# Kernel optimization log

Hardware: AMD Instinct MI355X
Metric: run time of the kernel (lower is better)

The kernel has to match this reference:

```python
import jax, jax.numpy as jnp
import numpy as np

B, N_CLS, A = 2, 3, 3
D = H = W = 96
K = 128
ALPHA = 1.0
EPS = 1e-4
BETA = 1.0 / 9
LAMB1 = LAMB2 = LAMB3 = 1.0


def setup_inputs() -> dict:
    key = jax.random.key(0)
    k1, k2, k3, k4, k5, k6, k7, k8 = jax.random.split(key, 8)
    cls_logit = jax.random.normal(k1, (B, N_CLS * A, D, H, W), jnp.float32)
    reg_pred = jax.random.normal(k2, (B, 6 * A, D, H, W), jnp.float32)

    def make_coord(ka, kd):
        ca = jax.random.randint(ka, (B, K, 1), 0, A)
        cs = jax.random.randint(kd, (B, K, 3), 0, D)
        c = jnp.concatenate([ca, cs], -1).astype(jnp.int32)
        valid = (jnp.arange(K) < (3 * K // 4))[None, :, None]
        return jnp.where(valid, c, -1)

    coord_prob = make_coord(k3, k4)
    coord_diff = make_coord(k5, k6)
    # class labels 1..N_CLS scattered into prob_gt at the positive coords; -1 elsewhere = negative
    cls_lab = jax.random.randint(k7, (B, K), 1, N_CLS + 1).astype(jnp.float32)
    prob_gt = -jnp.ones((B, A, D, H, W), jnp.float32)
    bidx = jnp.broadcast_to(jnp.arange(B)[:, None], (B, K))
    cc = jnp.maximum(coord_prob, 0)
    lab = jnp.where(coord_prob[:, :, 0] > -1, cls_lab, -1.0)
    prob_gt = prob_gt.at[bidx, cc[..., 0], cc[..., 1], cc[..., 2], cc[..., 3]].set(lab)
    diff_gt = jax.random.normal(k8, (B, K, 6), jnp.float32) * 0.1
    weight_cls = jnp.array([1.0, 2.0, 1.5], jnp.float32)  # [1] + cls_weight
    return {"cls_logit": cls_logit, "reg_pred": reg_pred, "prob_gt": prob_gt,
            "coord_prob": coord_prob, "coord_diff": coord_diff,
            "diff_gt": diff_gt, "weight_cls": weight_cls}


def _gather(x, c):
    # x: [C, A, D, H, W], c: [K, 4] -> [C, K]
    return x[:, c[:, 0], c[:, 1], c[:, 2], c[:, 3]]


def _smooth_l1(x, t):
    n = jnp.abs(x - t)
    return jnp.where(n < BETA, 0.5 * n * n / BETA, n - 0.5 * BETA)


def _forward(cls_logit, reg_pred, diff_gt, weight_cls, prob_gt, coord_prob, coord_diff):
    sg = jax.lax.stop_gradient
    prob = jnp.clip(jax.nn.sigmoid(cls_logit), EPS, 1.0 - EPS)  # [B, NC*A, D, H, W]

    # ---- negative focal loss with NMS-style peak filtering ----
    negmask = jnp.broadcast_to((prob_gt == -1.0).astype(jnp.float32)[:, None],
                               (B, N_CLS, A, D, H, W)).reshape(B, N_CLS * A, D, H, W)
    mp = jax.lax.reduce_window(cls_logit, -jnp.inf, jax.lax.max,
                               (1, 1, 3, 3, 3), (1, 1, 1, 1, 1),
                               [(0, 0), (0, 0), (1, 1), (1, 1), (1, 1)])
    negmask = negmask * (mp == cls_logit).astype(jnp.float32) * (prob > EPS).astype(jnp.float32)
    w_neg = sg(prob) ** ALPHA * negmask
    l_neg = -jnp.sum(jnp.log(1.0 - prob) * w_neg)
    count_neg = jnp.sum(w_neg)

    # ---- positive focal loss (masked fixed-K gather replaces ragged per-sample loop) ----
    p6 = prob.reshape(B, N_CLS, A, D, H, W)
    mask = (coord_prob[:, :, 0] > -1).astype(jnp.float32)  # [B, K]
    cc = jnp.maximum(coord_prob, 0)
    p_others = jax.vmap(_gather)(p6, cc)  # [B, NC, K]
    pg = jax.vmap(lambda p, c: p[c[:, 0], c[:, 1], c[:, 2], c[:, 3]])(prob_gt, cc)
    cls_gt = jnp.clip(pg.astype(jnp.int32) - 1, 0, N_CLS - 1)  # [B, K]
    p_target = jnp.take_along_axis(p_others, cls_gt[:, None, :], axis=1)[:, 0]  # [B, K]
    w_pos = sg(1.0 - p_target) ** ALPHA * weight_cls[cls_gt] * mask
    l_pos = -jnp.sum(jnp.log(p_target) * w_pos)
    count_pos = jnp.sum(w_pos)

    # ---- other-class suppression term ----
    is_tgt = jnp.arange(N_CLS)[None, :, None] == cls_gt[:, None, :]
    w_oth = (jax.nn.relu(p_others - (p_target - 0.1)[:, None, :])
             * (p_others > 0.5) * (p_target > 0.5)[:, None, :])
    w_oth = sg(jnp.where(is_tgt, 0.0, w_oth) * mask[:, None, :])
    l_other = jnp.sum(-jnp.log(1.0 - p_others) * w_oth)
    count_other = jnp.sum(w_oth)

    d6 = reg_pred.reshape(B, 6, A, D, H, W)
    mask_d = (coord_diff[:, :, 0] > -1).astype(jnp.float32)
    ccd = jnp.maximum(coord_diff, 0)
    d_samp = jnp.transpose(jax.vmap(_gather)(d6, ccd), (0, 2, 1))  # [B, K, 6]
    reg_loss = jnp.sum(_smooth_l1(d_samp, diff_gt) * mask_d[:, :, None])
    reg_weight = jnp.sum(mask_d)

    total = l_pos + l_neg * LAMB1 + l_other * LAMB3 + reg_loss * LAMB2
    return jnp.stack([total, l_pos, l_neg, l_other, reg_loss,
                      count_pos, count_neg, count_other, reg_weight])


def reference(cls_logit, reg_pred, prob_gt, coord_prob, coord_diff, diff_gt, weight_cls):
    return _forward(cls_logit, reg_pred, diff_gt, weight_cls, prob_gt, coord_prob, coord_diff)
```

## Files before the change

### kernel.cpp

```cpp
#include <hip/hip_runtime.h>
#include <cmath>

constexpr int B_ = 2, NCLS = 3, A_ = 3, D_ = 96, H_ = 96, W_ = 96, K_ = 128;
constexpr int CH = NCLS * A_;
constexpr int HW = H_ * W_;
constexpr int SPAT = D_ * HW;
constexpr float EPS_ = 1e-4f;
constexpr float BETA_ = 1.0f / 9.0f;

constexpr int WPL = 6;
constexpr int DCHUNK = 6;
constexpr int NDC = D_ / DCHUNK;
constexpr int HGRP = 4;
constexpr int NHG = H_ / HGRP;
constexpr int NWAVES = B_ * CH * NHG * NDC;
constexpr int NBLK = NWAVES / 4;

static __device__ __forceinline__ float sigmoid_clip(float x) {
  float s = 1.0f / (1.0f + __expf(-x));
  return fminf(fmaxf(s, EPS_), 1.0f - EPS_);
}

static __device__ __forceinline__ void load6(const float* __restrict__ p,
                                             float* f) {
  const float2 u0 = *(const float2*)(p);
  const float2 u1 = *(const float2*)(p + 2);
  const float2 u2 = *(const float2*)(p + 4);
  f[0] = u0.x; f[1] = u0.y; f[2] = u1.x;
  f[3] = u1.y; f[4] = u2.x; f[5] = u2.y;
}

__global__ __launch_bounds__(256) void neg_loss_kernel(
    const float* __restrict__ x, const float* __restrict__ pgt,
    float* __restrict__ ws) {
  const int tid = threadIdx.x;
  const int lane = tid & 63;
  int t = blockIdx.x * 4 + (tid >> 6);
  const int dci = t % NDC; t /= NDC;
  const int hg = t % NHG; t /= NHG;
  const int c = t % CH;
  const int b = t / CH;

  const int hl = lane >> 4;
  const int wseg = lane & 15;
  const int h = hg * HGRP + hl;
  const int w0 = wseg * WPL;
  const int d0 = dci * DCHUNK;
  const int a = c - (c / A_) * A_;

  const float* base = x + (size_t)(b * CH + c) * SPAT;
  const int hm = max(h - 1, 0), hq = min(h + 1, H_ - 1);
  const float* rowm = base + hm * W_ + w0;
  const float* rowc = base + h * W_ + w0;
  const float* rowp = base + hq * W_ + w0;
  const float* pgb = pgt + (size_t)(b * A_ + a) * SPAT + h * W_ + w0;

  float sprev[6], scur[6], ccur[6];
  float bufm[2][6], bufc[2][6], bufp[2][6];
  float pgbuf[2][6];
  {
    float fm[6], fc[6], fp[6], gm[6], gc[6], gp[6];
    const int plm = max(d0 - 1, 0) * HW;
    load6(rowm + plm, fm); load6(rowc + plm, fc); load6(rowp + plm, fp);
    const int pl0 = d0 * HW;
    load6(rowm + pl0, gm); load6(rowc + pl0, gc); load6(rowp + pl0, gp);
    const int pl1 = (d0 + 1) * HW;
    load6(rowm + pl1, bufm[0]); load6(rowc + pl1, bufc[0]);
    load6(rowp + pl1, bufp[0]);
    const int pl2 = (d0 + 2) * HW;
    load6(rowm + pl2, bufm[1]); load6(rowc + pl2, bufc[1]);
    load6(rowp + pl2, bufp[1]);
    load6(pgb + pl0, pgbuf[0]);
    load6(pgb + pl1, pgbuf[1]);
#pragma unroll
    for (int i = 0; i < 6; ++i) sprev[i] = fmaxf(fmaxf(fm[i], fc[i]), fp[i]);
#pragma unroll
    for (int i = 0; i < 6; ++i) {
      scur[i] = fmaxf(fmaxf(gm[i], gc[i]), gp[i]);
      ccur[i] = gc[i];
    }
  }

  float lsum = 0.0f, csum = 0.0f;
#pragma unroll
  for (int k = 0; k < DCHUNK; ++k) {
    const int d = d0 + k;
    const int par = k & 1;
    float snext[6], cnext[6], pgc[6];
#pragma unroll
    for (int i = 0; i < 6; ++i) {
      snext[i] = fmaxf(fmaxf(bufm[par][i], bufc[par][i]), bufp[par][i]);
      cnext[i] = bufc[par][i];
      pgc[i] = pgbuf[par][i];
    }
    const int pl3 = min(d + 3, D_ - 1) * HW;
    load6(rowm + pl3, bufm[par]); load6(rowc + pl3, bufc[par]);
    load6(rowp + pl3, bufp[par]);
    load6(pgb + min(d + 2, D_ - 1) * HW, pgbuf[par]);

    float cmx[6], m[6];
#pragma unroll
    for (int i = 0; i < 6; ++i)
      cmx[i] = fmaxf(fmaxf(sprev[i], scur[i]), snext[i]);
    float left = __shfl_up(cmx[5], 1);
    float right = __shfl_down(cmx[0], 1);
    if (wseg == 0) left = cmx[0];
    if (wseg == 15) right = cmx[5];
    m[0] = fmaxf(left, fmaxf(cmx[0], cmx[1]));
    m[1] = fmaxf(cmx[0], fmaxf(cmx[1], cmx[2]));
    m[2] = fmaxf(cmx[1], fmaxf(cmx[2], cmx[3]));
    m[3] = fmaxf(cmx[2], fmaxf(cmx[3], cmx[4]));
    m[4] = fmaxf(cmx[3], fmaxf(cmx[4], cmx[5]));
    m[5] = fmaxf(cmx[4], fmaxf(cmx[5], right));

#pragma unroll
    for (int i = 0; i < 6; ++i) {
      const float prob = sigmoid_clip(ccur[i]);
      const bool pred =
          (m[i] == ccur[i]) && (pgc[i] == -1.0f) && (prob > EPS_);
      lsum += pred ? (-__logf(1.0f - prob) * prob) : 0.0f;
      csum += pred ? prob : 0.0f;
    }
#pragma unroll
    for (int i = 0; i < 6; ++i) {
      sprev[i] = scur[i]; scur[i] = snext[i]; ccur[i] = cnext[i];
    }
  }

#pragma unroll
  for (int off = 32; off > 0; off >>= 1) {
    lsum += __shfl_down(lsum, off);
    csum += __shfl_down(csum, off);
  }
  __shared__ float sl[4], sc[4];
  const int wv = tid >> 6;
  if (lane == 0) { sl[wv] = lsum; sc[wv] = csum; }
  __syncthreads();
  if (tid == 0) {
    ws[blockIdx.x] = sl[0] + sl[1] + sl[2] + sl[3];
    ws[NBLK + blockIdx.x] = sc[0] + sc[1] + sc[2] + sc[3];
  }
}

__global__ __launch_bounds__(256) void small_kernel(
    const float* __restrict__ x, const float* __restrict__ rp,
    const float* __restrict__ pgt, const int* __restrict__ cprob,
    const int* __restrict__ cdiff, const float* __restrict__ dgt,
    const float* __restrict__ wcls, const float* __restrict__ ws,
    float* __restrict__ out) {
  const int tid = threadIdx.x;
  float v[8] = {0.f, 0.f, 0.f, 0.f, 0.f, 0.f, 0.f, 0.f};
  for (int i = tid; i < NBLK; i += 256) {
    v[6] += ws[i];
    v[7] += ws[NBLK + i];
  }
  if (tid < B_ * K_) {
    const int b = tid / K_, k = tid - b * K_;
    {
      const int* cp = cprob + (b * K_ + k) * 4;
      const int ca = cp[0];
      const float m = (ca > -1) ? 1.0f : 0.0f;
      const int a = max(ca, 0), d = max(cp[1], 0), h = max(cp[2], 0),
                ww = max(cp[3], 0);
      const int sp = (d * H_ + h) * W_ + ww;
      float po[NCLS];
#pragma unroll
      for (int c = 0; c < NCLS; ++c)
        po[c] = sigmoid_clip(x[(size_t)(b * CH + c * A_ + a) * SPAT + sp]);
      const float pg = pgt[(size_t)(b * A_ + a) * SPAT + sp];
      int cg = (int)pg - 1;
      cg = min(max(cg, 0), NCLS - 1);
      const float pt = po[cg];
      const float wp = (1.0f - pt) * wcls[cg] * m;
      v[0] = -__logf(pt) * wp;
      v[1] = wp;
      const float ptgt = (pt > 0.5f) ? 1.0f : 0.0f;
#pragma unroll
      for (int c = 0; c < NCLS; ++c) {
        if (c == cg) continue;
        const float wo = fmaxf(po[c] - (pt - 0.1f), 0.0f) *
                         ((po[c] > 0.5f) ? 1.0f : 0.0f) * ptgt * m;
        v[2] += -__logf(1.0f - po[c]) * wo;
        v[3] += wo;
      }
    }
    {
      const int* cd = cdiff + (b * K_ + k) * 4;
      const float md = (cd[0] > -1) ? 1.0f : 0.0f;
      const int a = max(cd[0], 0), d = max(cd[1], 0), h = max(cd[2], 0),
                ww = max(cd[3], 0);
      const int sp = (d * H_ + h) * W_ + ww;
#pragma unroll
      for (int j = 0; j < 6; ++j) {
        const float val = rp[(size_t)(b * 6 * A_ + j * A_ + a) * SPAT + sp];
        const float tgt = dgt[(b * K_ + k) * 6 + j];
        const float n = fabsf(val - tgt);
        const float s = (n < BETA_) ? (0.5f * n * n / BETA_) : (n - 0.5f * BETA_);
        v[4] += s * md;
      }
      v[5] = md;
    }
  }
  __shared__ float red[256][8];
#pragma unroll
  for (int j = 0; j < 8; ++j) red[tid][j] = v[j];
  __syncthreads();
  for (int s = 128; s > 0; s >>= 1) {
    if (tid < s) {
#pragma unroll
      for (int j = 0; j < 8; ++j) red[tid][j] += red[tid + s][j];
    }
    __syncthreads();
  }
  if (tid == 0) {
    const float l_pos = red[0][0], c_pos = red[0][1];
    const float l_oth = red[0][2], c_oth = red[0][3];
    const float l_reg = red[0][4], c_reg = red[0][5];
    const float l_neg = red[0][6], c_neg = red[0][7];
    out[0] = l_pos + l_neg + l_oth + l_reg;
    out[1] = l_pos;
    out[2] = l_neg;
    out[3] = l_oth;
    out[4] = l_reg;
    out[5] = c_pos;
    out[6] = c_neg;
    out[7] = c_oth;
    out[8] = c_reg;
  }
}

extern "C" void kernel_launch(void* const* d_in, const int* in_sizes, int n_in,
                              void* d_out, int out_size, void* d_ws,
                              size_t ws_size, hipStream_t stream) {
  const float* cls_logit = (const float*)d_in[0];
  const float* reg_pred = (const float*)d_in[1];
  const float* prob_gt = (const float*)d_in[2];
  const int* coord_prob = (const int*)d_in[3];
  const int* coord_diff = (const int*)d_in[4];
  const float* diff_gt = (const float*)d_in[5];
  const float* weight_cls = (const float*)d_in[6];
  float* out = (float*)d_out;
  float* ws = (float*)d_ws;

  neg_loss_kernel<<<NBLK, 256, 0, stream>>>(cls_logit, prob_gt, ws);
  small_kernel<<<1, 256, 0, stream>>>(cls_logit, reg_pred, prob_gt, coord_prob,
                                      coord_diff, diff_gt, weight_cls, ws,
                                      out);
}
```

Before: 231.3 us.

## Fuse gather losses and final reduction into neg-loss kernel via atomics

Merges the single-block gather/regression kernel into the main neg-loss kernel, with block 0 doing the positive, other-class and regression terms before its stencil work. Per-block partials are accumulated with float atomics, and a last-block-done counter writes the final outputs. This replaces a second kernel launch and its serial reduction over block partials with a memset plus atomic traffic. Block 0 now carries extra latency, and the atomic float summation order is nondeterministic.

```diff
diff --git a/kernel.cpp b/kernel.cpp
--- a/kernel.cpp
+++ b/kernel.cpp
@@ -16,6 +16,7 @@
 constexpr int NWAVES = B_ * CH * NHG * NDC;
 constexpr int NBLK = NWAVES / 4;
 
+
 static __device__ __forceinline__ float sigmoid_clip(float x) {
   float s = 1.0f / (1.0f + __expf(-x));
   return fminf(fmaxf(s, EPS_), 1.0f - EPS_);
@@ -30,11 +31,79 @@
   f[3] = u1.y; f[4] = u2.x; f[5] = u2.y;
 }
 
-__global__ __launch_bounds__(256) void neg_loss_kernel(
-    const float* __restrict__ x, const float* __restrict__ pgt,
-    float* __restrict__ ws) {
+__global__ __launch_bounds__(256) void ssd_loss_fused_kernel(
+    const float* __restrict__ x, const float* __restrict__ rp,
+    const float* __restrict__ pgt, const int* __restrict__ cprob,
+    const int* __restrict__ cdiff, const float* __restrict__ dgt,
+    const float* __restrict__ wcls, float* __restrict__ acc,
+    unsigned int* __restrict__ cnt, float* __restrict__ out) {
   const int tid = threadIdx.x;
   const int lane = tid & 63;
+
+  if (blockIdx.x == 0) {
+    float v[6] = {0.f, 0.f, 0.f, 0.f, 0.f, 0.f};
+    {
+      const int b = tid / K_, k = tid - b * K_;
+      {
+        const int* cp = cprob + (b * K_ + k) * 4;
+        const int ca = cp[0];
+        const float m = (ca > -1) ? 1.0f : 0.0f;
+        const int a = max(ca, 0), d = max(cp[1], 0), h = max(cp[2], 0),
+                  ww = max(cp[3], 0);
+        const int sp = (d * H_ + h) * W_ + ww;
+        float po[NCLS];
+#pragma unroll
+        for (int c = 0; c < NCLS; ++c)
+          po[c] = sigmoid_clip(x[(size_t)(b * CH + c * A_ + a) * SPAT + sp]);
+        const float pg = pgt[(size_t)(b * A_ + a) * SPAT + sp];
+        int cg = (int)pg - 1;
+        cg = min(max(cg, 0), NCLS - 1);
+        const float pt = po[cg];
+        const float wp = (1.0f - pt) * wcls[cg] * m;
+        v[0] = -__logf(pt) * wp;
+        v[1] = wp;
+        const float ptgt = (pt > 0.5f) ? 1.0f : 0.0f;
+#pragma unroll
+        for (int c = 0; c < NCLS; ++c) {
+          if (c == cg) continue;
+          const float wo = fmaxf(po[c] - (pt - 0.1f), 0.0f) *
+                           ((po[c] > 0.5f) ? 1.0f : 0.0f) * ptgt * m;
+          v[2] += -__logf(1.0f - po[c]) * wo;
+          v[3] += wo;
+        }
+      }
+      {
+        const int* cd = cdiff + (b * K_ + k) * 4;
+        const float md = (cd[0] > -1) ? 1.0f : 0.0f;
+        const int a = max(cd[0], 0), d = max(cd[1], 0), h = max(cd[2], 0),
+                  ww = max(cd[3], 0);
+        const int sp = (d * H_ + h) * W_ + ww;
+#pragma unroll
+        for (int j = 0; j < 6; ++j) {
+          const float val = rp[(size_t)(b * 6 * A_ + j * A_ + a) * SPAT + sp];
+          const float tgt = dgt[(b * K_ + k) * 6 + j];
+          const float n = fabsf(val - tgt);
+          const float s =
+              (n < BETA_) ? (0.5f * n * n / BETA_) : (n - 0.5f * BETA_);
+          v[4] += s * md;
+        }
+        v[5] = md;
+      }
+    }
+    __shared__ float red[256][6];
+#pragma unroll
+    for (int j = 0; j < 6; ++j) red[tid][j] = v[j];
+    __syncthreads();
+    for (int s = 128; s > 0; s >>= 1) {
+      if (tid < s) {
+#pragma unroll
+        for (int j = 0; j < 6; ++j) red[tid][j] += red[tid + s][j];
+      }
+      __syncthreads();
+    }
+    if (tid < 6) atomicAdd(&acc[2 + tid], red[0][tid]);
+  }
+
   int t = blockIdx.x * 4 + (tid >> 6);
   const int dci = t % NDC; t /= NDC;
   const int hg = t % NHG; t /= NHG;
@@ -137,95 +206,28 @@
   if (lane == 0) { sl[wv] = lsum; sc[wv] = csum; }
   __syncthreads();
   if (tid == 0) {
-    ws[blockIdx.x] = sl[0] + sl[1] + sl[2] + sl[3];
-    ws[NBLK + blockIdx.x] = sc[0] + sc[1] + sc[2] + sc[3];
-  }
-}
-
-__global__ __launch_bounds__(256) void small_kernel(
-    const float* __restrict__ x, const float* __restrict__ rp,
-    const float* __restrict__ pgt, const int* __restrict__ cprob,
-    const int* __restrict__ cdiff, const float* __restrict__ dgt,
-    const float* __restrict__ wcls, const float* __restrict__ ws,
-    float* __restrict__ out) {
-  const int tid = threadIdx.x;
-  float v[8] = {0.f, 0.f, 0.f, 0.f, 0.f, 0.f, 0.f, 0.f};
-  for (int i = tid; i < NBLK; i += 256) {
-    v[6] += ws[i];
-    v[7] += ws[NBLK + i];
-  }
-  if (tid < B_ * K_) {
-    const int b = tid / K_, k = tid - b * K_;
-    {
-      const int* cp = cprob + (b * K_ + k) * 4;
-      const int ca = cp[0];
-      const float m = (ca > -1) ? 1.0f : 0.0f;
-      const int a = max(ca, 0), d = max(cp[1], 0), h = max(cp[2], 0),
-                ww = max(cp[3], 0);
-      const int sp = (d * H_ + h) * W_ + ww;
-      float po[NCLS];
-#pragma unroll
-      for (int c = 0; c < NCLS; ++c)
-        po[c] = sigmoid_clip(x[(size_t)(b * CH + c * A_ + a) * SPAT + sp]);
-      const float pg = pgt[(size_t)(b * A_ + a) * SPAT + sp];
-      int cg = (int)pg - 1;
-      cg = min(max(cg, 0), NCLS - 1);
-      const float pt = po[cg];
-      const float wp = (1.0f - pt) * wcls[cg] * m;
-      v[0] = -__logf(pt) * wp;
-      v[1] = wp;
-      const float ptgt = (pt > 0.5f) ? 1.0f : 0.0f;
-#pragma unroll
-      for (int c = 0; c < NCLS; ++c) {
-        if (c == cg) continue;
-        const float wo = fmaxf(po[c] - (pt - 0.1f), 0.0f) *
-                         ((po[c] > 0.5f) ? 1.0f : 0.0f) * ptgt * m;
-        v[2] += -__logf(1.0f - po[c]) * wo;
-        v[3] += wo;
-      }
-    }
-    {
-      const int* cd = cdiff + (b * K_ + k) * 4;
-      const float md = (cd[0] > -1) ? 1.0f : 0.0f;
-      const int a = max(cd[0], 0), d = max(cd[1], 0), h = max(cd[2], 0),
-                ww = max(cd[3], 0);
-      const int sp = (d * H_ + h) * W_ + ww;
-#pragma unroll
-      for (int j = 0; j < 6; ++j) {
-        const float val = rp[(size_t)(b * 6 * A_ + j * A_ + a) * SPAT + sp];
-        const float tgt = dgt[(b * K_ + k) * 6 + j];
-        const float n = fabsf(val - tgt);
-        const float s = (n < BETA_) ? (0.5f * n * n / BETA_) : (n - 0.5f * BETA_);
-        v[4] += s * md;
-      }
-      v[5] = md;
-    }
-  }
-  __shared__ float red[256][8];
-#pragma unroll
-  for (int j = 0; j < 8; ++j) red[tid][j] = v[j];
-  __syncthreads();
-  for (int s = 128; s > 0; s >>= 1) {
-    if (tid < s) {
-#pragma unroll
-      for (int j = 0; j < 8; ++j) red[tid][j] += red[tid + s][j];
-    }
-    __syncthreads();
-  }
-  if (tid == 0) {
-    const float l_pos = red[0][0], c_pos = red[0][1];
-    const float l_oth = red[0][2], c_oth = red[0][3];
-    const float l_reg = red[0][4], c_reg = red[0][5];
-    const float l_neg = red[0][6], c_neg = red[0][7];
-    out[0] = l_pos + l_neg + l_oth + l_reg;
-    out[1] = l_pos;
-    out[2] = l_neg;
-    out[3] = l_oth;
-    out[4] = l_reg;
-    out[5] = c_pos;
-    out[6] = c_neg;
-    out[7] = c_oth;
-    out[8] = c_reg;
+    atomicAdd(&acc[0], sl[0] + sl[1] + sl[2] + sl[3]);
+    atomicAdd(&acc[1], sc[0] + sc[1] + sc[2] + sc[3]);
+    __threadfence();
+    const unsigned int old = atomicAdd(cnt, 1u);
+    if (old == (unsigned int)(NBLK - 1)) {
+      float av[8];
+#pragma unroll
+      for (int j = 0; j < 8; ++j) av[j] = atomicAdd(&acc[j], 0.0f);
+      const float l_neg = av[0], c_neg = av[1];
+      const float l_pos = av[2], c_pos = av[3];
+      const float l_oth = av[4], c_oth = av[5];
+      const float l_reg = av[6], c_reg = av[7];
+      out[0] = l_pos + l_neg + l_oth + l_reg;
+      out[1] = l_pos;
+      out[2] = l_neg;
+      out[3] = l_oth;
+      out[4] = l_reg;
+      out[5] = c_pos;
+      out[6] = c_neg;
+      out[7] = c_oth;
+      out[8] = c_reg;
+    }
   }
 }
 
@@ -240,10 +242,11 @@
   const float* diff_gt = (const float*)d_in[5];
   const float* weight_cls = (const float*)d_in[6];
   float* out = (float*)d_out;
-  float* ws = (float*)d_ws;
-
-  neg_loss_kernel<<<NBLK, 256, 0, stream>>>(cls_logit, prob_gt, ws);
-  small_kernel<<<1, 256, 0, stream>>>(cls_logit, reg_pred, prob_gt, coord_prob,
-                                      coord_diff, diff_gt, weight_cls, ws,
-                                      out);
-}
+  float* acc = (float*)d_ws;
+  unsigned int* cnt = (unsigned int*)(acc + 8);
+
+  hipMemsetAsync(d_ws, 0, 9 * sizeof(float), stream);
+  ssd_loss_fused_kernel<<<NBLK, 256, 0, stream>>>(
+      cls_logit, reg_pred, prob_gt, coord_prob, coord_diff, diff_gt,
+      weight_cls, acc, cnt, out);
+}
```

After: 305.7 us. +32.2%, slower.
